# Optimization experiments

Measured on AMD Instinct MI355X. Metric: run time of the kernel, lower is better.

The kernel has to match this reference:

```python
import jax, jax.numpy as jnp
import numpy as np

B, S, E, H = 2, 2048, 2048, 16
D = E // H  # head_dim = 128
MASKED_BIAS = -1e9


def setup_inputs() -> dict:
    key = jax.random.key(0)
    ks = jax.random.split(key, 5)
    scale = 0.02
    return {
        "hidden_states": jax.random.normal(ks[0], (B, S, E), dtype=jnp.float32),
        "Wq": jax.random.normal(ks[1], (E, E), dtype=jnp.float32) * scale,
        "Wk": jax.random.normal(ks[2], (E, E), dtype=jnp.float32) * scale,
        "Wv": jax.random.normal(ks[3], (E, E), dtype=jnp.float32) * scale,
        "Wo": jax.random.normal(ks[4], (E, E), dtype=jnp.float32) * scale,
        "bo": jnp.zeros((E,), dtype=jnp.float32),
    }


def reference(hidden_states, Wq, Wk, Wv, Wo, bo):
    x = hidden_states
    # torch Linear: y = x @ W.T (no bias for q/k/v)
    q = jnp.einsum("bse,fe->bsf", x, Wq).reshape(B, S, H, D).transpose(0, 2, 1, 3)
    k = jnp.einsum("bse,fe->bsf", x, Wk).reshape(B, S, H, D).transpose(0, 2, 1, 3)
    v = jnp.einsum("bse,fe->bsf", x, Wv).reshape(B, S, H, D).transpose(0, 2, 1, 3)
    # GPT-Neo: NO 1/sqrt(d) scaling, attention computed in fp32
    scores = jnp.einsum("bhqd,bhkd->bhqk", q.astype(jnp.float32), k.astype(jnp.float32))
    causal = jnp.tril(jnp.ones((S, S), dtype=bool))[None, None]
    scores = jnp.where(causal, scores, jnp.float32(MASKED_BIAS))
    weights = jax.nn.softmax(scores, axis=-1).astype(v.dtype)
    attn = jnp.einsum("bhqk,bhkd->bhqd", weights, v)
    attn = attn.transpose(0, 2, 1, 3).reshape(B, S, E)
    out = jnp.einsum("bse,fe->bsf", attn, Wo) + bo
    return out
```

## Files before the change

### kernel.cpp

```cpp
#include <hip/hip_runtime.h>
#include <stdint.h>
#include <stddef.h>

#define Bd 2
#define Sd 2048
#define Ed 2048
#define Hd 16
#define Dd 128

typedef unsigned short u16;
typedef _Float16 f16;
typedef __attribute__((ext_vector_type(8))) _Float16 half8;
typedef __attribute__((ext_vector_type(4))) float f32x4;

__device__ __forceinline__ u16 f2h(float f) {
  f16 h = (f16)f; return __builtin_bit_cast(u16, h);
}
__device__ __forceinline__ void gll16(const void* g, void* lds) {
  __builtin_amdgcn_global_load_lds(
      (const __attribute__((address_space(1))) void*)g,
      (__attribute__((address_space(3))) void*)lds, 16, 0, 0);
}
template<int C> __device__ __forceinline__ float dppmv(float x) {
  return __builtin_bit_cast(float,
      __builtin_amdgcn_update_dpp(0, __builtin_bit_cast(int, x), C, 0xF, 0xF, false));
}
__device__ __forceinline__ float rmax16(float x) {
  x = fmaxf(x, dppmv<0x121>(x)); x = fmaxf(x, dppmv<0x122>(x));
  x = fmaxf(x, dppmv<0x124>(x)); x = fmaxf(x, dppmv<0x128>(x));
  return x;
}
__device__ __forceinline__ float rsum16(float x) {
  x += dppmv<0x121>(x); x += dppmv<0x122>(x);
  x += dppmv<0x124>(x); x += dppmv<0x128>(x);
  return x;
}
#define MFMA(a,b,c) __builtin_amdgcn_mfma_f32_16x16x32_f16((a),(b),(c),0,0,0)

#define BARRIER() do { __builtin_amdgcn_s_barrier(); __builtin_amdgcn_sched_barrier(0); } while (0)
#define LGKM(n) do { asm volatile("s_waitcnt lgkmcnt(" #n ")" ::: "memory"); __builtin_amdgcn_sched_barrier(0); } while (0)
#define VMCNT(n) do { asm volatile("s_waitcnt vmcnt(" #n ")" ::: "memory"); __builtin_amdgcn_sched_barrier(0); } while (0)

__global__ void k_cvt5(const float* __restrict__ x,
                       const float* __restrict__ Wq, const float* __restrict__ Wk,
                       const float* __restrict__ Wv, const float* __restrict__ Wo,
                       u16* __restrict__ xh, u16* __restrict__ wq, u16* __restrict__ wk,
                       u16* __restrict__ wv, u16* __restrict__ wo) {
  const int stride = gridDim.x * blockDim.x;
  for (int i = blockIdx.x * blockDim.x + threadIdx.x; i < 6291456; i += stride) {
    const float* s; u16* d; int j;
    if (i < 2097152) { s = x; d = xh; j = i; }
    else {
      const int t = (i - 2097152) >> 20;
      j = (i - 2097152) & 1048575;
      s = (t == 0) ? Wq : (t == 1) ? Wk : (t == 2) ? Wv : Wo;
      d = (t == 0) ? wq : (t == 1) ? wk : (t == 2) ? wv : wo;
    }
    const float4 v = ((const float4*)s)[j];
    ((ushort4*)d)[j] = make_ushort4(f2h(v.x), f2h(v.y), f2h(v.z), f2h(v.w));
  }
}

__global__ __launch_bounds__(512, 2) void gemm_qk(
    const u16* __restrict__ xh,
    const u16* __restrict__ wq, const u16* __restrict__ wk,
    u16* __restrict__ Qf, u16* __restrict__ Kf) {
  constexpr int NT = 32;
  __shared__ __align__(16) char smem[131072];
  const int lin = blockIdx.x;
  const int z = lin >> 7;
  const int rr = lin & 127;
  const int n0 = (rr & 7) * 256;
  const int m0 = (rr >> 3) * 256;
  const u16* wgt = z ? wk : wq;
  u16* oq = z ? Kf : Qf;
  const int tid = threadIdx.x, wv = tid >> 6, ln = tid & 63;
  const int wvm = wv >> 2, wvn = wv & 3;

  auto stgA = [&](int tt, int par) {
    if (tt >= NT) return;
    const int kin = tt << 6;
    const int c = tt & 1;
    const int r8 = ln >> 3, cc = ((ln & 7) ^ r8) * 16;
#pragma unroll
    for (int e = 0; e < 2; ++e) {
      const int ch = e * 8 + wv;
      const int trow = (par + (ch >> 3) * 2) * 64 + (ch & 7) * 8;
      gll16((const char*)xh + (size_t)(m0 + trow + r8) * 4096 + (size_t)kin * 2 + cc,
            smem + c * 65536 + trow * 128);
    }
  };
  auto stgB = [&](int tt, int n2) {
    if (tt >= NT) return;
    const int kin = tt << 6;
    const int c = tt & 1;
    const int r8 = ln >> 3, cc = ((ln & 7) ^ r8) * 16;
#pragma unroll
    for (int e = 0; e < 2; ++e) {
      const int ch = e * 8 + wv;
      const int trow = (ch >> 2) * 64 + n2 * 32 + (ch & 3) * 8;
      gll16((const char*)wgt + (size_t)(n0 + trow + r8) * 4096 + (size_t)kin * 2 + cc,
            smem + c * 65536 + 32768 + trow * 128);
    }
  };
  auto ldAh = [&](int c, int h, half8 (*a)[2]) {
#pragma unroll
    for (int mm = 0; mm < 4; ++mm) {
      const int row = wvm * 128 + h * 64 + mm * 16 + (ln & 15);
#pragma unroll
      for (int s = 0; s < 2; ++s) {
        const int cb = (s * 64 + (ln >> 4) * 16) ^ ((row & 7) << 4);
        a[mm][s] = *(const half8*)(smem + c * 65536 + row * 128 + cb);
      }
    }
  };
  auto ldBh = [&](int c, int n2, half8 (*b)[2]) {
#pragma unroll
    for (int nn = 0; nn < 2; ++nn) {
      const int row = wvn * 64 + (n2 * 2 + nn) * 16 + (ln & 15);
#pragma unroll
      for (int s = 0; s < 2; ++s) {
        const int cb = (s * 64 + (ln >> 4) * 16) ^ ((row & 7) << 4);
        b[nn][s] = *(const half8*)(smem + c * 65536 + 32768 + row * 128 + cb);
      }
    }
  };

  const f32x4 fz = {0.f, 0.f, 0.f, 0.f};
  f32x4 acc[8][4];
#pragma unroll
  for (int mm = 0; mm < 8; ++mm)
#pragma unroll
    for (int nn = 0; nn < 4; ++nn) acc[mm][nn] = fz;

#define QUAD(MB, NB, AA, BB)                                                    \
  do {                                                                          \
    __builtin_amdgcn_s_setprio(1);                                              \
    _Pragma("unroll")                                                           \
    for (int mm = 0; mm < 4; ++mm)                                              \
      _Pragma("unroll")                                                         \
      for (int nn = 0; nn < 2; ++nn) {                                          \
        acc[MB + mm][NB + nn] = MFMA(AA[mm][0], BB[nn][0], acc[MB + mm][NB + nn]); \
        acc[MB + mm][NB + nn] = MFMA(AA[mm][1], BB[nn][1], acc[MB + mm][NB + nn]); \
      }                                                                         \
    __builtin_amdgcn_s_setprio(0);                                              \
  } while (0)

  stgA(0, 0); stgA(0, 1); stgB(0, 0); stgB(0, 1);
  stgA(1, 0); stgB(1, 0); stgB(1, 1);
  VMCNT(6);
  BARRIER();

  for (int w = 0; w < NT; ++w) {
    const int c = w & 1;
    half8 a[4][2], b0[2][2], b1[2][2];
    ldAh(c, 0, a);
    ldBh(c, 0, b0);
    stgA(w + 1, 1);
    BARRIER(); LGKM(0);
    QUAD(0, 0, a, b0);
    BARRIER();
    ldBh(c, 1, b1);
    stgA(w + 2, 0);
    BARRIER(); LGKM(0);
    QUAD(0, 2, a, b1);
    BARRIER();
    ldAh(c, 1, a);
    stgB(w + 2, 0);
    BARRIER(); LGKM(0);
    QUAD(4, 0, a, b0);
    BARRIER();
    stgB(w + 2, 1);
    BARRIER();
    QUAD(4, 2, a, b1);
    if (w + 2 < NT) { VMCNT(6); } else { VMCNT(0); }
    BARRIER();
  }
#undef QUAD

#pragma unroll
  for (int mm = 0; mm < 8; ++mm)
#pragma unroll
    for (int nn = 0; nn < 4; ++nn)
#pragma unroll
      for (int r4 = 0; r4 < 4; ++r4) {
        const int mg = m0 + wvm * 128 + mm * 16 + (ln >> 4) * 4 + r4;
        const int f = n0 + wvn * 64 + nn * 16 + (ln & 15);
        const int b = mg >> 11, s = mg & (Sd - 1);
        const int h = f >> 7, d = f & (Dd - 1);
        oq[(((size_t)b * Hd + h) * Sd + s) * Dd + d] = f2h(acc[mm][nn][r4]);
      }
}

template<int MODE>
__global__ __launch_bounds__(512, 2) void gemm1(
    const u16* __restrict__ Ap, const u16* __restrict__ Bp,
    const float* __restrict__ bias, u16* __restrict__ ob, float* __restrict__ of) {
  constexpr int NT = 32;
  __shared__ __align__(16) char smem[98304];
  const int bid = blockIdx.x;
  const int n0 = (bid & 7) * 256;
  const int m0 = (bid >> 3) * 128;
  const int tid = threadIdx.x, wv = tid >> 6, ln = tid & 63;
  const int wvm = wv >> 2, wvn = wv & 3;

  auto stageA = [&](int tt, int c) {
    const int kin = tt << 6;
#pragma unroll
    for (int i = 0; i < 2; ++i) {
      const int l2 = i * 8192 + wv * 1024 + ln * 16;
      const int row = l2 >> 7, cb = l2 & 127;
      const int gc = cb ^ ((row & 7) << 4);
      gll16((const char*)Ap + (size_t)(m0 + row) * 4096 + (size_t)kin * 2 + gc,
            smem + c * 49152 + i * 8192 + wv * 1024);
    }
  };
  auto stageB = [&](int tt, int c) {
    const int kin = tt << 6;
#pragma unroll
    for (int i = 0; i < 4; ++i) {
      const int l2 = i * 8192 + wv * 1024 + ln * 16;
      const int row = l2 >> 7, cb = l2 & 127;
      const int gc = cb ^ ((row & 7) << 4);
      gll16((const char*)Bp + (size_t)(n0 + row) * 4096 + (size_t)kin * 2 + gc,
            smem + c * 49152 + 16384 + i * 8192 + wv * 1024);
    }
  };
  auto ldA = [&](int c, int s, half8* af) {
#pragma unroll
    for (int mm = 0; mm < 4; ++mm) {
      const int row = wvm * 64 + mm * 16 + (ln & 15);
      const int cb = (s * 64 + (ln >> 4) * 16) ^ ((row & 7) << 4);
      af[mm] = *(const half8*)(smem + c * 49152 + row * 128 + cb);
    }
  };
  auto ldB = [&](int c, int s, int p, half8* bf) {
#pragma unroll
    for (int j = 0; j < 2; ++j) {
      const int row = wvn * 64 + (p * 2 + j) * 16 + (ln & 15);
      const int cb = (s * 64 + (ln >> 4) * 16) ^ ((row & 7) << 4);
      bf[j] = *(const half8*)(smem + c * 49152 + 16384 + row * 128 + cb);
    }
  };

  const f32x4 fz = {0.f, 0.f, 0.f, 0.f};
  f32x4 acc[4][4];
#pragma unroll
  for (int mm = 0; mm < 4; ++mm)
#pragma unroll
    for (int nn = 0; nn < 4; ++nn) acc[mm][nn] = fz;

  stageA(0, 0);
  stageB(0, 0);
  stageA(1, 1);
  VMCNT(2);
  BARRIER();

  for (int t = 0; t < NT; ++t) {
    const int c = t & 1;
    const bool h1 = (t + 1 < NT), h2 = (t + 2 < NT);
    half8 af[4], bf01[2], bf23[2];
    ldA(c, 0, af);
    ldB(c, 0, 0, bf01);
    ldB(c, 0, 1, bf23);
    if (h1) stageB(t + 1, c ^ 1);
    BARRIER();
    LGKM(2);
    __builtin_amdgcn_s_setprio(1);
#pragma unroll
    for (int mm = 0; mm < 4; ++mm) {
      acc[mm][0] = MFMA(af[mm], bf01[0], acc[mm][0]);
      acc[mm][1] = MFMA(af[mm], bf01[1], acc[mm][1]);
    }
    __builtin_amdgcn_s_setprio(0);
    BARRIER();
    LGKM(0);
    __builtin_amdgcn_s_setprio(1);
#pragma unroll
    for (int mm = 0; mm < 4; ++mm) {
      acc[mm][2] = MFMA(af[mm], bf23[0], acc[mm][2]);
      acc[mm][3] = MFMA(af[mm], bf23[1], acc[mm][3]);
    }
    __builtin_amdgcn_s_setprio(0);
    BARRIER();
    ldA(c, 1, af);
    ldB(c, 1, 0, bf01);
    ldB(c, 1, 1, bf23);
    BARRIER();
    LGKM(2);
    __builtin_amdgcn_s_setprio(1);
#pragma unroll
    for (int mm = 0; mm < 4; ++mm) {
      acc[mm][0] = MFMA(af[mm], bf01[0], acc[mm][0]);
      acc[mm][1] = MFMA(af[mm], bf01[1], acc[mm][1]);
    }
    __builtin_amdgcn_s_setprio(0);
    BARRIER();
    if (h2) stageA(t + 2, c);
    LGKM(0);
    __builtin_amdgcn_s_setprio(1);
#pragma unroll
    for (int mm = 0; mm < 4; ++mm) {
      acc[mm][2] = MFMA(af[mm], bf23[0], acc[mm][2]);
      acc[mm][3] = MFMA(af[mm], bf23[1], acc[mm][3]);
    }
    __builtin_amdgcn_s_setprio(0);
    if (h2)      { VMCNT(2); }
    else if (h1) { VMCNT(0); }
    BARRIER();
  }

#pragma unroll
  for (int mm = 0; mm < 4; ++mm)
#pragma unroll
    for (int nn = 0; nn < 4; ++nn) {
      const int f = n0 + wvn * 64 + nn * 16 + (ln & 15);
      float bi = 0.f;
      if (MODE == 1) bi = bias[f];
#pragma unroll
      for (int r4 = 0; r4 < 4; ++r4) {
        const int mg = m0 + wvm * 64 + mm * 16 + (ln >> 4) * 4 + r4;
        if (MODE == 0) {
          const int b = mg >> 11, s = mg & (Sd - 1);
          const int h = f >> 7, d = f & (Dd - 1);
          ob[(((size_t)b * Hd + h) * Sd + s) * Dd + d] = f2h(acc[mm][nn][r4]);
        } else {
          of[(size_t)mg * Ed + f] = acc[mm][nn][r4] + bi;
        }
      }
    }
}

__global__ __launch_bounds__(256, 2) void k_attn(
    const u16* __restrict__ Qf, const u16* __restrict__ Kf,
    const u16* __restrict__ Vb, u16* __restrict__ ctx) {
  __shared__ __align__(16) char smem[53248];
  char* KsB = smem;
  char* VtB = smem + 16384;
  char* PlB = smem + 34816;

  const int bh = blockIdx.x;
  const int qt = (int)gridDim.y - 1 - blockIdx.y;
  const int tid = threadIdx.x, wv = tid >> 6, ln = tid & 63;
  const int q0 = qt * 128 + wv * 32;
  const size_t headoff = (size_t)bh * Sd * Dd;

  half8 qf[2][4];
#pragma unroll
  for (int mi = 0; mi < 2; ++mi)
#pragma unroll
    for (int c = 0; c < 4; ++c) {
      const size_t off = headoff + (size_t)(q0 + mi * 16 + (ln & 15)) * Dd + c * 32 + (ln >> 4) * 8;
      qf[mi][c] = *(const half8*)(Qf + off);
    }

  const f32x4 fz = {0.f, 0.f, 0.f, 0.f};
  f32x4 acc_o[2][8];
  float m_run[2][4], l_run[2][4];
#pragma unroll
  for (int mi = 0; mi < 2; ++mi) {
#pragma unroll
    for (int n = 0; n < 8; ++n) acc_o[mi][n] = fz;
#pragma unroll
    for (int r = 0; r < 4; ++r) { m_run[mi][r] = -1e30f; l_run[mi][r] = 0.f; }
  }

  const int ktmax = 2 * qt + 1;
  for (int kt = 0; kt <= ktmax; ++kt) {
    const size_t ktile = (headoff + (size_t)kt * 64 * Dd) * 2;
#pragma unroll
    for (int i = 0; i < 4; ++i) {
      const int lin = i * 4096 + wv * 1024 + ln * 16;
      const int row = lin >> 8;
      const int cb = lin & 255;
      const int gc = cb ^ ((row & 7) << 4);
      gll16((const char*)Kf + ktile + (size_t)row * 256 + gc, KsB + i * 4096 + wv * 1024);
    }
#pragma unroll
    for (int p = 0; p < 4; ++p) {
      const int rr = (tid >> 4) + 16 * p;
      const int d0 = (tid & 15) * 8;
      const ushort4 vv0 = *(const ushort4*)(Vb + headoff + (size_t)(kt * 64 + rr) * Dd + d0);
      const ushort4 vv1 = *(const ushort4*)(Vb + headoff + (size_t)(kt * 64 + rr) * Dd + d0 + 4);
      const u16 vs[8] = {vv0.x, vv0.y, vv0.z, vv0.w, vv1.x, vv1.y, vv1.z, vv1.w};
#pragma unroll
      for (int j = 0; j < 8; ++j) {
        const int d = d0 + j;
        *(u16*)(VtB + d * 144 + ((rr * 2) ^ (((d >> 3) & 7) << 4))) = vs[j];
      }
    }
    __syncthreads();

    const bool skip = (kt * 64) > (q0 + 31);

    f32x4 sc[2][4];
#pragma unroll
    for (int mi = 0; mi < 2; ++mi)
#pragma unroll
      for (int t = 0; t < 4; ++t) sc[mi][t] = fz;
    if (!skip) {
#pragma unroll
      for (int t = 0; t < 4; ++t)
#pragma unroll
        for (int c = 0; c < 4; ++c) {
          const int row = t * 16 + (ln & 15);
          const int cb = (c * 64 + (ln >> 4) * 16) ^ ((row & 7) << 4);
          const half8 kh8 = *(const half8*)(KsB + row * 256 + cb);
#pragma unroll
          for (int mi = 0; mi < 2; ++mi)
            sc[mi][t] = MFMA(qf[mi][c], kh8, sc[mi][t]);
        }
      if (kt >= 2 * qt) {
#pragma unroll
        for (int mi = 0; mi < 2; ++mi)
#pragma unroll
          for (int t = 0; t < 4; ++t)
#pragma unroll
            for (int r = 0; r < 4; ++r) {
              const int qg = q0 + mi * 16 + (ln >> 4) * 4 + r;
              const int kg = kt * 64 + t * 16 + (ln & 15);
              if (kg > qg) sc[mi][t][r] = -1e30f;
            }
      }

#pragma unroll
      for (int mi = 0; mi < 2; ++mi)
#pragma unroll
        for (int r = 0; r < 4; ++r) {
          float rm = fmaxf(fmaxf(sc[mi][0][r], sc[mi][1][r]),
                           fmaxf(sc[mi][2][r], sc[mi][3][r]));
          rm = rmax16(rm);
          const float mn = fmaxf(m_run[mi][r], rm);
          const float alpha = __expf(m_run[mi][r] - mn);
          m_run[mi][r] = mn;
          const int irow = mi * 16 + (ln >> 4) * 4 + r;
          float ps = 0.f;
#pragma unroll
          for (int t = 0; t < 4; ++t) {
            const float pv = __expf(sc[mi][t][r] - mn);
            ps += pv;
            *(u16*)(PlB + wv * 4608 + irow * 144 + (t * 16 + (ln & 15)) * 2) = f2h(pv);
          }
          ps = rsum16(ps);
          l_run[mi][r] = l_run[mi][r] * alpha + ps;
#pragma unroll
          for (int n = 0; n < 8; ++n) acc_o[mi][n][r] *= alpha;
        }
    }
    asm volatile("s_waitcnt lgkmcnt(0)" ::: "memory");
    __builtin_amdgcn_sched_barrier(0);

    if (!skip) {
      half8 pf[2][2];
#pragma unroll
      for (int mi = 0; mi < 2; ++mi)
#pragma unroll
        for (int c2 = 0; c2 < 2; ++c2)
          pf[mi][c2] = *(const half8*)(PlB + wv * 4608 + (mi * 16 + (ln & 15)) * 144 +
                                       c2 * 64 + (ln >> 4) * 16);
#pragma unroll
      for (int n = 0; n < 8; ++n)
#pragma unroll
        for (int c2 = 0; c2 < 2; ++c2) {
          const int d = n * 16 + (ln & 15);
          const half8 v8 = *(const half8*)(VtB + d * 144 +
                             ((c2 * 64 + (ln >> 4) * 16) ^ (((d >> 3) & 7) << 4)));
          acc_o[0][n] = MFMA(pf[0][c2], v8, acc_o[0][n]);
          acc_o[1][n] = MFMA(pf[1][c2], v8, acc_o[1][n]);
        }
    }
    __syncthreads();
  }

  const int b = bh >> 4, h = bh & 15;
#pragma unroll
  for (int mi = 0; mi < 2; ++mi)
#pragma unroll
    for (int r = 0; r < 4; ++r) {
      const float inv = 1.f / l_run[mi][r];
      const int s = q0 + mi * 16 + (ln >> 4) * 4 + r;
#pragma unroll
      for (int n = 0; n < 8; ++n) {
        const int col = n * 16 + (ln & 15);
        ctx[((size_t)b * Sd + s) * Ed + h * Dd + col] = f2h(acc_o[mi][n][r] * inv);
      }
    }
}

extern "C" void kernel_launch(void* const* d_in, const int* in_sizes, int n_in,
                              void* d_out, int out_size, void* d_ws, size_t ws_size,
                              hipStream_t stream) {
  (void)in_sizes; (void)n_in; (void)out_size; (void)ws_size;
  const float* x  = (const float*)d_in[0];
  const float* Wq = (const float*)d_in[1];
  const float* Wk = (const float*)d_in[2];
  const float* Wv = (const float*)d_in[3];
  const float* Wo = (const float*)d_in[4];
  const float* bo = (const float*)d_in[5];
  float* out = (float*)d_out;

  const size_t NTOK = (size_t)Bd * Sd * Ed;
  const size_t NW   = (size_t)Ed * Ed;

  char* w = (char*)d_ws;
  u16* xh  = (u16*)w; w += NTOK * 2;
  u16* wq  = (u16*)w; w += NW * 2;
  u16* wk  = (u16*)w; w += NW * 2;
  u16* wv  = (u16*)w; w += NW * 2;
  u16* wo  = (u16*)w; w += NW * 2;
  u16* Qf  = (u16*)w; w += NTOK * 2;
  u16* Kf  = (u16*)w; w += NTOK * 2;
  u16* Vf  = (u16*)w; w += NTOK * 2;
  u16* ctx = (u16*)w; w += NTOK * 2;

  k_cvt5<<<dim3(2048), 256, 0, stream>>>(x, Wq, Wk, Wv, Wo, xh, wq, wk, wv, wo);

  gemm_qk<<<dim3(256), 512, 0, stream>>>(xh, wq, wk, Qf, Kf);
  gemm1<0><<<dim3(256), 512, 0, stream>>>(xh, wv, nullptr, Vf, nullptr);

  k_attn<<<dim3(Bd * Hd, Sd / 128), 256, 0, stream>>>(Qf, Kf, Vf, ctx);

  gemm1<1><<<dim3(256), 512, 0, stream>>>(ctx, wo, bo, nullptr, out);
}
```

Baseline: 258.3 us.

## Double-buffer K tiles, prefetch V into registers, add lazy softmax rescale

K tiles are now double-buffered in LDS and the next K/V tile is prefetched during the current iteration's compute, with V held in registers and transposed into LDS after the PV step. A lazy online-softmax rescale skips the max update and accumulator rescaling unless some row's max grows by more than 8. The causal q-tile order is also changed to pair short and long tiles across blockIdx.y. This adds LDS use (69 KB), an extra barrier per iteration, and more register pressure at 2 blocks per CU.

```diff
diff --git a/kernel.cpp b/kernel.cpp
--- a/kernel.cpp
+++ b/kernel.cpp
@@ -334,13 +334,13 @@
 __global__ __launch_bounds__(256, 2) void k_attn(
     const u16* __restrict__ Qf, const u16* __restrict__ Kf,
     const u16* __restrict__ Vb, u16* __restrict__ ctx) {
-  __shared__ __align__(16) char smem[53248];
-  char* KsB = smem;
-  char* VtB = smem + 16384;
-  char* PlB = smem + 34816;
+  __shared__ __align__(16) char smem[69632];
+  char* VtB = smem + 32768;
+  char* PlB = smem + 51200;
 
   const int bh = blockIdx.x;
-  const int qt = (int)gridDim.y - 1 - blockIdx.y;
+  const int y = blockIdx.y;
+  const int qt = (y < 8) ? y : (23 - y);
   const int tid = threadIdx.x, wv = tid >> 6, ln = tid & 63;
   const int q0 = qt * 128 + wv * 32;
   const size_t headoff = (size_t)bh * Sd * Dd;
@@ -365,47 +365,71 @@
     for (int r = 0; r < 4; ++r) { m_run[mi][r] = -1e30f; l_run[mi][r] = 0.f; }
   }
 
-  const int ktmax = 2 * qt + 1;
-  for (int kt = 0; kt <= ktmax; ++kt) {
+  uint4 vpre[4];
+  auto stageK = [&](int kt, int c) {
     const size_t ktile = (headoff + (size_t)kt * 64 * Dd) * 2;
 #pragma unroll
     for (int i = 0; i < 4; ++i) {
-      const int lin = i * 4096 + wv * 1024 + ln * 16;
-      const int row = lin >> 8;
-      const int cb = lin & 255;
+      const int l2 = i * 4096 + wv * 1024 + ln * 16;
+      const int row = l2 >> 8;
+      const int cb = l2 & 255;
       const int gc = cb ^ ((row & 7) << 4);
-      gll16((const char*)Kf + ktile + (size_t)row * 256 + gc, KsB + i * 4096 + wv * 1024);
-    }
+      gll16((const char*)Kf + ktile + (size_t)row * 256 + gc,
+            smem + c * 16384 + i * 4096 + wv * 1024);
+    }
+  };
+  auto loadV = [&](int kt) {
+#pragma unroll
+    for (int p = 0; p < 4; ++p) {
+      const int rr = (tid >> 4) + 16 * p;
+      vpre[p] = *(const uint4*)(Vb + headoff + (size_t)(kt * 64 + rr) * Dd + (tid & 15) * 8);
+    }
+  };
+  auto writeV = [&]() {
 #pragma unroll
     for (int p = 0; p < 4; ++p) {
       const int rr = (tid >> 4) + 16 * p;
       const int d0 = (tid & 15) * 8;
-      const ushort4 vv0 = *(const ushort4*)(Vb + headoff + (size_t)(kt * 64 + rr) * Dd + d0);
-      const ushort4 vv1 = *(const ushort4*)(Vb + headoff + (size_t)(kt * 64 + rr) * Dd + d0 + 4);
-      const u16 vs[8] = {vv0.x, vv0.y, vv0.z, vv0.w, vv1.x, vv1.y, vv1.z, vv1.w};
+      const u16 es[8] = {(u16)(vpre[p].x & 0xffff), (u16)(vpre[p].x >> 16),
+                         (u16)(vpre[p].y & 0xffff), (u16)(vpre[p].y >> 16),
+                         (u16)(vpre[p].z & 0xffff), (u16)(vpre[p].z >> 16),
+                         (u16)(vpre[p].w & 0xffff), (u16)(vpre[p].w >> 16)};
 #pragma unroll
       for (int j = 0; j < 8; ++j) {
         const int d = d0 + j;
-        *(u16*)(VtB + d * 144 + ((rr * 2) ^ (((d >> 3) & 7) << 4))) = vs[j];
-      }
-    }
-    __syncthreads();
+        *(u16*)(VtB + d * 144 + ((rr * 2) ^ (((d >> 3) & 7) << 4))) = es[j];
+      }
+    }
+  };
+
+  const int ktmax = 2 * qt + 1;
+  stageK(0, 0);
+  loadV(0);
+  VMCNT(0);
+  writeV();
+  BARRIER();
+
+  for (int kt = 0; kt <= ktmax; ++kt) {
+    const int cur = kt & 1;
+    const bool more = (kt < ktmax);
+    if (more) { stageK(kt + 1, cur ^ 1); loadV(kt + 1); }
+    __builtin_amdgcn_sched_barrier(0);
 
     const bool skip = (kt * 64) > (q0 + 31);
 
-    f32x4 sc[2][4];
-#pragma unroll
-    for (int mi = 0; mi < 2; ++mi)
-#pragma unroll
-      for (int t = 0; t < 4; ++t) sc[mi][t] = fz;
     if (!skip) {
+      f32x4 sc[2][4];
+#pragma unroll
+      for (int mi = 0; mi < 2; ++mi)
+#pragma unroll
+        for (int t = 0; t < 4; ++t) sc[mi][t] = fz;
 #pragma unroll
       for (int t = 0; t < 4; ++t)
 #pragma unroll
         for (int c = 0; c < 4; ++c) {
           const int row = t * 16 + (ln & 15);
           const int cb = (c * 64 + (ln >> 4) * 16) ^ ((row & 7) << 4);
-          const half8 kh8 = *(const half8*)(KsB + row * 256 + cb);
+          const half8 kh8 = *(const half8*)(smem + cur * 16384 + row * 256 + cb);
 #pragma unroll
           for (int mi = 0; mi < 2; ++mi)
             sc[mi][t] = MFMA(qf[mi][c], kh8, sc[mi][t]);
@@ -423,6 +447,8 @@
             }
       }
 
+      float rm_[2][4];
+      bool flag = false;
 #pragma unroll
       for (int mi = 0; mi < 2; ++mi)
 #pragma unroll
@@ -430,25 +456,50 @@
           float rm = fmaxf(fmaxf(sc[mi][0][r], sc[mi][1][r]),
                            fmaxf(sc[mi][2][r], sc[mi][3][r]));
           rm = rmax16(rm);
-          const float mn = fmaxf(m_run[mi][r], rm);
-          const float alpha = __expf(m_run[mi][r] - mn);
-          m_run[mi][r] = mn;
-          const int irow = mi * 16 + (ln >> 4) * 4 + r;
-          float ps = 0.f;
-#pragma unroll
-          for (int t = 0; t < 4; ++t) {
-            const float pv = __expf(sc[mi][t][r] - mn);
-            ps += pv;
-            *(u16*)(PlB + wv * 4608 + irow * 144 + (t * 16 + (ln & 15)) * 2) = f2h(pv);
+          rm_[mi][r] = rm;
+          flag |= (rm > m_run[mi][r] + 8.f);
+        }
+      if (__ballot(flag) != 0ull) {
+#pragma unroll
+        for (int mi = 0; mi < 2; ++mi)
+#pragma unroll
+          for (int r = 0; r < 4; ++r) {
+            const float mn = fmaxf(m_run[mi][r], rm_[mi][r]);
+            const float alpha = __expf(m_run[mi][r] - mn);
+            m_run[mi][r] = mn;
+            const int irow = mi * 16 + (ln >> 4) * 4 + r;
+            float ps = 0.f;
+#pragma unroll
+            for (int t = 0; t < 4; ++t) {
+              const float pv = __expf(sc[mi][t][r] - mn);
+              ps += pv;
+              *(u16*)(PlB + wv * 4608 + irow * 144 + (t * 16 + (ln & 15)) * 2) = f2h(pv);
+            }
+            ps = rsum16(ps);
+            l_run[mi][r] = l_run[mi][r] * alpha + ps;
+#pragma unroll
+            for (int n = 0; n < 8; ++n) acc_o[mi][n][r] *= alpha;
           }
-          ps = rsum16(ps);
-          l_run[mi][r] = l_run[mi][r] * alpha + ps;
-#pragma unroll
-          for (int n = 0; n < 8; ++n) acc_o[mi][n][r] *= alpha;
-        }
-    }
-    asm volatile("s_waitcnt lgkmcnt(0)" ::: "memory");
-    __builtin_amdgcn_sched_barrier(0);
+      } else {
+#pragma unroll
+        for (int mi = 0; mi < 2; ++mi)
+#pragma unroll
+          for (int r = 0; r < 4; ++r) {
+            const float mn = m_run[mi][r];
+            const int irow = mi * 16 + (ln >> 4) * 4 + r;
+            float ps = 0.f;
+#pragma unroll
+            for (int t = 0; t < 4; ++t) {
+              const float pv = __expf(sc[mi][t][r] - mn);
+              ps += pv;
+              *(u16*)(PlB + wv * 4608 + irow * 144 + (t * 16 + (ln & 15)) * 2) = f2h(pv);
+            }
+            ps = rsum16(ps);
+            l_run[mi][r] += ps;
+          }
+      }
+    }
+    LGKM(0);
 
     if (!skip) {
       half8 pf[2][2];
@@ -469,7 +520,12 @@
           acc_o[1][n] = MFMA(pf[1][c2], v8, acc_o[1][n]);
         }
     }
-    __syncthreads();
+    BARRIER();
+    if (more) {
+      VMCNT(0);
+      writeV();
+    }
+    BARRIER();
   }
 
   const int b = bh >> 4, h = bh & 15;
```

Result: slower. 322.6 us (+24.9%).
